# Optimization experiments

Measured on AMD Instinct MI355X. Metric: run time of the kernel, lower is better.

The kernel has to match this reference:

```python
import jax, jax.numpy as jnp
import numpy as np

OUT = 7   # output_size
SR = 2    # sampling_ratio
SCALES = (0.25, 0.125, 0.0625, 0.03125)  # inferred from feat sizes vs 800x800 image
K_MIN, LVL0, S0, EPS = 2, 4.0, 224.0, 1e-6


def _bilinear_gather(feat, b, y, x):
    """Legacy (aligned=False) bilinear sampling. feat [B,C,H,W]; b,y,x same shape S.
    Returns [*S, C]."""
    B, C, H, W = feat.shape
    valid = (y >= -1.0) & (y <= H) & (x >= -1.0) & (x <= W)
    y = jnp.maximum(y, 0.0)
    x = jnp.maximum(x, 0.0)
    yl = y.astype(jnp.int32)
    xl = x.astype(jnp.int32)
    ycond = yl >= H - 1
    yl = jnp.where(ycond, H - 1, yl)
    yh = jnp.where(ycond, H - 1, yl + 1)
    y = jnp.where(ycond, yl.astype(y.dtype), y)
    xcond = xl >= W - 1
    xl = jnp.where(xcond, W - 1, xl)
    xh = jnp.where(xcond, W - 1, xl + 1)
    x = jnp.where(xcond, xl.astype(x.dtype), x)
    ly = y - yl
    lx = x - xl
    hy = 1.0 - ly
    hx = 1.0 - lx
    def g(yy, xx):
        return feat[b, :, yy, xx]  # advanced indexing -> [*S, C]
    val = ((hy * hx)[..., None] * g(yl, xl)
           + (hy * lx)[..., None] * g(yl, xh)
           + (ly * hx)[..., None] * g(yh, xl)
           + (ly * lx)[..., None] * g(yh, xh))
    return jnp.where(valid[..., None], val, 0.0)


def _roi_align(feat, bidx, boxes, scale):
    """RoIAlign (aligned=False). feat [B,C,H,W], bidx [R] int, boxes [R,4] image coords.
    Returns [R,C,OUT,OUT]."""
    x1 = boxes[:, 0] * scale
    y1 = boxes[:, 1] * scale
    x2 = boxes[:, 2] * scale
    y2 = boxes[:, 3] * scale
    roi_w = jnp.maximum(x2 - x1, 1.0)
    roi_h = jnp.maximum(y2 - y1, 1.0)
    bin_h = roi_h / OUT
    bin_w = roi_w / OUT
    off = (jnp.arange(SR, dtype=feat.dtype) + 0.5) / SR      # [SR]
    ph = jnp.arange(OUT, dtype=feat.dtype)                   # [OUT]
    grid = ph[None, :, None] + off[None, None, :]            # [1,OUT,SR]
    ys = y1[:, None, None] + grid * bin_h[:, None, None]     # [R,OUT,SR]
    xs = x1[:, None, None] + grid * bin_w[:, None, None]     # [R,OUT,SR]
    Y = ys[:, :, None, :, None]                              # [R,OUT,1,SR,1]
    X = xs[:, None, :, None, :]                              # [R,1,OUT,1,SR]
    Yb, Xb = jnp.broadcast_arrays(Y, X)                      # [R,OUT,OUT,SR,SR]
    b = jnp.broadcast_to(bidx[:, None, None, None, None], Yb.shape)
    val = _bilinear_gather(feat, b, Yb, Xb)                  # [R,OUT,OUT,SR,SR,C]
    pooled = val.mean(axis=(3, 4))                           # [R,OUT,OUT,C]
    return jnp.transpose(pooled, (0, 3, 1, 2))               # [R,C,OUT,OUT]


def _levels(boxes_flat):
    """LevelMapper.run: FPN level index (0-based) per RoI."""
    area = (boxes_flat[:, 2] - boxes_flat[:, 0]) * (boxes_flat[:, 3] - boxes_flat[:, 1])
    s = jnp.sqrt(area)
    lvl = jnp.floor(LVL0 + jnp.log2(s / S0 + EPS))
    return jnp.clip(lvl, K_MIN, K_MIN + 3).astype(jnp.int32) - K_MIN


def setup_inputs() -> dict:
    key = jax.random.key(0)
    ks = jax.random.split(key, 6)
    sizes = [200, 100, 50, 25]
    inp = {f"feat{i}": jax.random.normal(ks[i], (2, 256, s, s), dtype=jnp.float32)
           for i, s in enumerate(sizes)}
    xy = jax.random.uniform(ks[4], (2, 256, 2), dtype=jnp.float32) * 500.0
    wh = jax.random.uniform(ks[5], (2, 256, 2), dtype=jnp.float32) * 400.0 + 8.0
    inp["boxes"] = jnp.concatenate([xy, xy + wh], axis=-1)  # (x1,y1,x2,y2) in [0,908)
    return inp


def reference(feat0, feat1, feat2, feat3, boxes):
    feats = [feat0, feat1, feat2, feat3]
    B, N, _ = boxes.shape
    bf = boxes.reshape(B * N, 4)
    bidx = jnp.repeat(jnp.arange(B, dtype=jnp.int32), N)  # convert_to_roi_format ids
    lv = _levels(bf)
    C = feats[0].shape[1]
    out = jnp.zeros((B * N, C, OUT, OUT), dtype=feats[0].dtype)
    for level, (f, sc) in enumerate(zip(feats, SCALES)):
        r = _roi_align(f, bidx, bf, sc)
        out = jnp.where((lv == level)[:, None, None, None], r, out)
    return out
```

## Files before the change

### kernel.cpp

```cpp
#include <hip/hip_runtime.h>

#define OUT 7
#define NCH 256
#define NROI 512
#define NS 14
#define NT 28
#define CCH 16
#define W9 9
#define WPC 253
#define TPR (NCH * OUT * OUT)

__device__ __forceinline__ float rfl_f(float v) {
    return __int_as_float(__builtin_amdgcn_readfirstlane(__float_as_int(v)));
}

__device__ __forceinline__ unsigned short f2bf_rne(float f) {
    unsigned int u = __float_as_uint(f);
    u += 0x7FFFu + ((u >> 16) & 1u);
    return (unsigned short)(u >> 16);
}

__global__ __launch_bounds__(256, 4) void roi_align_tap16_kernel(
        const float* __restrict__ f0, const float* __restrict__ f1,
        const float* __restrict__ f2, const float* __restrict__ f3,
        const float* __restrict__ boxes, float* __restrict__ out) {
    __shared__ unsigned short sm[NT * WPC * 2];
    __shared__ int   rowIdx[NT];
    __shared__ int   colIdx[NT];
    __shared__ float lyS[NS], vyS[NS], lxS[NS], vxS[NS];

    int g    = blockIdx.x;
    int xcd  = g & 7;
    int slot = g >> 3;
    int rr   = slot >> 4;
    int q    = slot & 15;
    int r    = rr * 8 + xcd;
    int tid  = (int)threadIdx.x;

    float bx1 = rfl_f(boxes[r * 4 + 0]);
    float by1 = rfl_f(boxes[r * 4 + 1]);
    float bx2 = rfl_f(boxes[r * 4 + 2]);
    float by2 = rfl_f(boxes[r * 4 + 3]);

    float area = (bx2 - bx1) * (by2 - by1);
    float s    = sqrtf(area);
    float lvl  = floorf(4.0f + log2f(s * (1.0f / 224.0f) + 1e-6f));
    lvl        = fminf(fmaxf(lvl, 2.0f), 5.0f);
    int level  = __builtin_amdgcn_readfirstlane((int)lvl - 2);

    const float* f; int H; float scale;
    switch (level) {
        case 0:  f = f0; H = 200; scale = 0.25f;    break;
        case 1:  f = f1; H = 100; scale = 0.125f;   break;
        case 2:  f = f2; H = 50;  scale = 0.0625f;  break;
        default: f = f3; H = 25;  scale = 0.03125f; break;
    }
    float Hf = (float)H;

    float x1 = bx1 * scale, y1 = by1 * scale;
    float roi_w = fmaxf(bx2 * scale - x1, 1.0f);
    float roi_h = fmaxf(by2 * scale - y1, 1.0f);
    float bin_w = roi_w * (1.0f / OUT);
    float bin_h = roi_h * (1.0f / OUT);

    if (tid < NS) {
        int ph = tid >> 1, iy = tid & 1;
        float y = y1 + ((float)ph + (iy ? 0.75f : 0.25f)) * bin_h;
        float v = (y >= -1.0f && y <= Hf) ? 0.5f : 0.0f;
        y = fmaxf(y, 0.0f);
        int yl = (int)y, yh;
        float ly;
        if (yl >= H - 1) { yl = H - 1; yh = H - 1; ly = 0.0f; }
        else             { yh = yl + 1; ly = y - (float)yl; }
        lyS[tid] = ly; vyS[tid] = v;
        rowIdx[2 * tid]     = yl;
        rowIdx[2 * tid + 1] = yh;
    } else if (tid >= 32 && tid < 32 + NS) {
        int t = tid - 32;
        int pw = t >> 1, ix = t & 1;
        float x = x1 + ((float)pw + (ix ? 0.75f : 0.25f)) * bin_w;
        float v = (x >= -1.0f && x <= Hf) ? 0.5f : 0.0f;
        x = fmaxf(x, 0.0f);
        int xl = (int)x, xh;
        float lx;
        if (xl >= H - 1) { xl = H - 1; xh = H - 1; lx = 0.0f; }
        else             { xh = xl + 1; lx = x - (float)xl; }
        lxS[t] = lx; vxS[t] = v;
        colIdx[2 * t]     = xl;
        colIdx[2 * t + 1] = xh;
    }
    __syncthreads();

    int bidx = r >> 8;
    size_t HH = (size_t)(H * H);
    const float* plane = f + (size_t)(bidx * NCH + q * CCH) * HH;

    int lane = tid & 63;
    int wave = tid >> 6;
    int  j   = (lane < 28) ? lane : ((lane < 56) ? lane - 28 : lane - 56);
    int  cg  = (lane >= 28 && lane < 56) ? 1 : 0;
    bool act = (lane < 56);
    int  col = colIdx[j];

#pragma unroll
    for (int t = 0; t < 7; ++t) {
        int rs = wave * 7 + t;
        size_t rbase = (size_t)rowIdx[rs] * (size_t)H + (size_t)col;
        float v[8];
#pragma unroll
        for (int cc = 0; cc < 8; ++cc)
            v[cc] = plane[(size_t)(cg * 8 + cc) * HH + rbase];
        unsigned short* dstp = sm + (j * WPC + rs * W9) * 2 + cg * 8;
#pragma unroll
        for (int cc = 0; cc < 8; ++cc)
            if (act) dstp[cc] = f2bf_rne(v[cc]);
    }
    __syncthreads();

    const unsigned int* smw = (const unsigned int*)sm;
    float accx[2], accy[2];
#pragma unroll
    for (int i = 0; i < 2; ++i) { accx[i] = 0.0f; accy[i] = 0.0f; }

#pragma unroll
    for (int i = 0; i < 2; ++i) {
        int o = tid + 256 * i;
        if (o < 392) {
            int cp = o & 7, px = o >> 3;
            int ph = px / 7, pw = px - ph * 7;
            float ax = 0.0f, ay = 0.0f;
#pragma unroll
            for (int iy = 0; iy < 2; ++iy) {
                int sy = ph * 2 + iy;
                float ly = lyS[sy], hy = 1.0f - ly;
                float vy = vyS[sy];
                int r0 = (2 * sy) * W9 + cp;
                int r1 = r0 + W9;
#pragma unroll
                for (int ix = 0; ix < 2; ++ix) {
                    int sx = pw * 2 + ix;
                    float lx = lxS[sx], hx = 1.0f - lx;
                    float m  = vy * vxS[sx];
                    int c0 = (2 * sx) * WPC;
                    int c1 = c0 + WPC;
                    unsigned int u00 = smw[c0 + r0];
                    unsigned int u01 = smw[c1 + r0];
                    unsigned int u10 = smw[c0 + r1];
                    unsigned int u11 = smw[c1 + r1];
                    float w00 = hy * hx * m, w01 = hy * lx * m;
                    float w10 = ly * hx * m, w11 = ly * lx * m;
                    ax = fmaf(w00, __uint_as_float(u00 << 16), ax);
                    ay = fmaf(w00, __uint_as_float(u00 & 0xFFFF0000u), ay);
                    ax = fmaf(w01, __uint_as_float(u01 << 16), ax);
                    ay = fmaf(w01, __uint_as_float(u01 & 0xFFFF0000u), ay);
                    ax = fmaf(w10, __uint_as_float(u10 << 16), ax);
                    ay = fmaf(w10, __uint_as_float(u10 & 0xFFFF0000u), ay);
                    ax = fmaf(w11, __uint_as_float(u11 << 16), ax);
                    ay = fmaf(w11, __uint_as_float(u11 & 0xFFFF0000u), ay);
                }
            }
            accx[i] = ax; accy[i] = ay;
        }
    }
    __syncthreads();

    float* smf = (float*)sm;
#pragma unroll
    for (int i = 0; i < 2; ++i) {
        int o = tid + 256 * i;
        if (o < 392) {
            int cp = o & 7, px = o >> 3;
            smf[(cp * 2 + 0) * 49 + px] = accx[i];
            smf[(cp * 2 + 1) * 49 + px] = accy[i];
        }
    }
    __syncthreads();

    float* dst = out + (size_t)r * TPR + (size_t)q * (CCH * 49);
    for (int e = tid; e < CCH * 49; e += 256) dst[e] = smf[e];
}

extern "C" void kernel_launch(void* const* d_in, const int* in_sizes, int n_in,
                              void* d_out, int out_size, void* d_ws, size_t ws_size,
                              hipStream_t stream) {
    const float* f0    = (const float*)d_in[0];
    const float* f1    = (const float*)d_in[1];
    const float* f2    = (const float*)d_in[2];
    const float* f3    = (const float*)d_in[3];
    const float* boxes = (const float*)d_in[4];
    float* out         = (float*)d_out;

    roi_align_tap16_kernel<<<NROI * 16, 256, 0, stream>>>(f0, f1, f2, f3, boxes, out);
}
```

Measured before the change: 182.2 us.

## Deduplicate contiguous ROI row/col taps before staging features into shared memory

Before staging, the kernel checks whether the 28 row (or column) sample indices of an ROI cover a contiguous range of at most 28 distinct pixels. If so, it loads only that unique range and remaps the bilinear reads through rowMap/colMap tables. This removes redundant global loads for small ROIs where taps overlap. In exchange it adds an extra sync, a runtime loop bound in place of the unrolled loop, and indirection in the compute phase. Launch bounds also rise to 5 blocks per SM.

```diff
diff --git a/kernel.cpp b/kernel.cpp
--- a/kernel.cpp
+++ b/kernel.cpp
@@ -20,13 +20,15 @@
     return (unsigned short)(u >> 16);
 }
 
-__global__ __launch_bounds__(256, 4) void roi_align_tap16_kernel(
+__global__ __launch_bounds__(256, 5) void roi_align_tap16d_kernel(
         const float* __restrict__ f0, const float* __restrict__ f1,
         const float* __restrict__ f2, const float* __restrict__ f3,
         const float* __restrict__ boxes, float* __restrict__ out) {
     __shared__ unsigned short sm[NT * WPC * 2];
-    __shared__ int   rowIdx[NT];
-    __shared__ int   colIdx[NT];
+    __shared__ int   rowIdx[NT], colIdx[NT];
+    __shared__ int   rowSt[NT],  colSt[NT];
+    __shared__ int   rowMap[NT], colMap[NT];
+    __shared__ int   NRC[2];
     __shared__ float lyS[NS], vyS[NS], lxS[NS], vxS[NS];
 
     int g    = blockIdx.x;
@@ -91,21 +93,39 @@
     }
     __syncthreads();
 
+    if (tid < NT) {
+        int rmin = rowIdx[0], rmax = rowIdx[NT - 1];
+        int range = rmax - rmin + 1;
+        bool cont = (range <= NT);
+        rowSt[tid]  = cont ? min(rmin + tid, rmax) : rowIdx[tid];
+        rowMap[tid] = cont ? (rowIdx[tid] - rmin) : tid;
+        if (tid == 0) NRC[0] = cont ? range : NT;
+    } else if (tid >= 64 && tid < 64 + NT) {
+        int t = tid - 64;
+        int cmin = colIdx[0], cmax = colIdx[NT - 1];
+        int range = cmax - cmin + 1;
+        bool cont = (range <= NT);
+        colSt[t]  = cont ? min(cmin + t, cmax) : colIdx[t];
+        colMap[t] = cont ? (colIdx[t] - cmin) : t;
+        if (t == 0) NRC[1] = cont ? range : NT;
+    }
+    __syncthreads();
+
     int bidx = r >> 8;
     size_t HH = (size_t)(H * H);
     const float* plane = f + (size_t)(bidx * NCH + q * CCH) * HH;
 
+    int NR = NRC[0], NC = NRC[1];
     int lane = tid & 63;
     int wave = tid >> 6;
-    int  j   = (lane < 28) ? lane : ((lane < 56) ? lane - 28 : lane - 56);
-    int  cg  = (lane >= 28 && lane < 56) ? 1 : 0;
-    bool act = (lane < 56);
-    int  col = colIdx[j];
-
-#pragma unroll
-    for (int t = 0; t < 7; ++t) {
-        int rs = wave * 7 + t;
-        size_t rbase = (size_t)rowIdx[rs] * (size_t)H + (size_t)col;
+    int  j    = (lane < NT) ? lane : ((lane < 2 * NT) ? lane - NT : 0);
+    int  cg   = (lane >= NT && lane < 2 * NT) ? 1 : 0;
+    bool act0 = (lane < 2 * NT);
+    int  col  = colSt[j];
+
+    for (int rs = wave; rs < NR; rs += 4) {
+        bool act = act0 && (j < NC);
+        size_t rbase = (size_t)rowSt[rs] * (size_t)H + (size_t)col;
         float v[8];
 #pragma unroll
         for (int cc = 0; cc < 8; ++cc)
@@ -134,15 +154,15 @@
                 int sy = ph * 2 + iy;
                 float ly = lyS[sy], hy = 1.0f - ly;
                 float vy = vyS[sy];
-                int r0 = (2 * sy) * W9 + cp;
-                int r1 = r0 + W9;
+                int r0 = rowMap[2 * sy]     * W9 + cp;
+                int r1 = rowMap[2 * sy + 1] * W9 + cp;
 #pragma unroll
                 for (int ix = 0; ix < 2; ++ix) {
                     int sx = pw * 2 + ix;
                     float lx = lxS[sx], hx = 1.0f - lx;
                     float m  = vy * vxS[sx];
-                    int c0 = (2 * sx) * WPC;
-                    int c1 = c0 + WPC;
+                    int c0 = colMap[2 * sx]     * WPC;
+                    int c1 = colMap[2 * sx + 1] * WPC;
                     unsigned int u00 = smw[c0 + r0];
                     unsigned int u01 = smw[c1 + r0];
                     unsigned int u10 = smw[c0 + r1];
@@ -190,5 +210,5 @@
     const float* boxes = (const float*)d_in[4];
     float* out         = (float*)d_out;
 
-    roi_align_tap16_kernel<<<NROI * 16, 256, 0, stream>>>(f0, f1, f2, f3, boxes, out);
-}
+    roi_align_tap16d_kernel<<<NROI * 16, 256, 0, stream>>>(f0, f1, f2, f3, boxes, out);
+}
```

Measured after the change: 183.6 us. About the same (+0.8%).
